# Kernel tuning notes

Hardware: AMD Instinct MI355X
Metric: run time of the kernel (lower is better)

The kernel has to match this reference:

```python
import jax, jax.numpy as jnp
import numpy as np


def bitnet_quantize(w):
    # scale = mean(|w|) clamped; ternary round of centered/scaled weights; STE
    scale = jnp.maximum(jnp.mean(jnp.abs(w)), 1e-8)
    w_centered = w - jnp.mean(w)
    w_bin = jnp.round(jnp.clip(w_centered / scale, -1.0, 1.0))
    w_q = jax.lax.stop_gradient(w_bin - w) + w  # forward: w_bin, grad: identity
    return w_q, scale


def setup_inputs() -> dict:
    key = jax.random.key(0)
    kx, kr, ki, kj, kk = jax.random.split(key, 5)
    B, S, F = 4, 4096, 2048
    C = F // 4  # 512 quaternion channels
    init_std = 0.02
    return {
        "x": jax.random.normal(kx, (B, S, F), dtype=jnp.float32),
        "r_weight": jax.random.normal(kr, (C, C), dtype=jnp.float32) * init_std,
        "i_weight": jax.random.normal(ki, (C, C), dtype=jnp.float32) * init_std,
        "j_weight": jax.random.normal(kj, (C, C), dtype=jnp.float32) * init_std,
        "k_weight": jax.random.normal(kk, (C, C), dtype=jnp.float32) * init_std,
        "bias": jnp.zeros((F,), dtype=jnp.float32),
    }


def reference(x, r_weight, i_weight, j_weight, k_weight, bias):
    # eval path of QuatBitLinear: ternary-quantize all 4 weights, shared scale
    r_w, s1 = bitnet_quantize(r_weight)
    i_w, s2 = bitnet_quantize(i_weight)
    j_w, s3 = bitnet_quantize(j_weight)
    k_w, s4 = bitnet_quantize(k_weight)
    scale = (s1 + s2 + s3 + s4) / 4.0

    r_in, i_in, j_in, k_in = jnp.split(x, 4, axis=-1)  # each [B,S,C]

    def lin(v, w):  # F.linear: v @ w.T
        return jnp.einsum('bsc,oc->bso', v, w)

    r_out = lin(r_in, r_w) - lin(i_in, i_w) - lin(j_in, j_w) - lin(k_in, k_w)
    i_out = lin(r_in, i_w) + lin(i_in, r_w) + lin(j_in, k_w) - lin(k_in, j_w)
    j_out = lin(r_in, j_w) - lin(i_in, k_w) + lin(j_in, r_w) + lin(k_in, i_w)
    k_out = lin(r_in, k_w) + lin(i_in, j_w) - lin(j_in, i_w) + lin(k_in, r_w)

    out = jnp.concatenate([r_out, i_out, j_out, k_out], axis=-1)
    out = out + bias  # bias added BEFORE scaling, as in the torch code
    return out * scale * 0.5
```

## Files before the change

### kernel.cpp

```cpp
#include <hip/hip_runtime.h>
#include <hip/hip_bf16.h>
#include <stdint.h>

typedef __attribute__((ext_vector_type(8))) short short8;
typedef __attribute__((ext_vector_type(4))) float f32x4;
typedef __attribute__((ext_vector_type(4))) float float4v;
typedef __attribute__((ext_vector_type(4))) unsigned short ushort4v;

static constexpr int C = 512;
static constexpr int F = 2048;
static constexpr int NW = C * C;

__device__ inline unsigned short f2bf(float f) {
    union { float f; unsigned int u; } cv;
    cv.f = f;
    unsigned int r = cv.u + 0x7fffu + ((cv.u >> 16) & 1u);
    return (unsigned short)(r >> 16);
}

__global__ void qb_sums(const float* __restrict__ w0, const float* __restrict__ w1,
                        const float* __restrict__ w2, const float* __restrict__ w3,
                        double* __restrict__ sums) {
    int wid = blockIdx.x >> 6;
    int chunk = blockIdx.x & 63;
    const float* wsel = (wid == 0) ? w0 : (wid == 1) ? w1 : (wid == 2) ? w2 : w3;
    const float* p = wsel + chunk * (NW / 64);
    double sa = 0.0, sv = 0.0;
    for (int i = threadIdx.x; i < (NW / 64) / 4; i += 256) {
        float4v v = ((const float4v*)p)[i];
        sa += (double)fabsf(v.x) + fabsf(v.y) + fabsf(v.z) + fabsf(v.w);
        sv += (double)v.x + v.y + v.z + v.w;
    }
    for (int off = 32; off; off >>= 1) {
        sa += __shfl_down(sa, off);
        sv += __shfl_down(sv, off);
    }
    __shared__ double red[8];
    int wv = threadIdx.x >> 6;
    if ((threadIdx.x & 63) == 0) { red[wv] = sa; red[4 + wv] = sv; }
    __syncthreads();
    if (threadIdx.x == 0) {
        double tsa = red[0] + red[1] + red[2] + red[3];
        double tsv = red[4] + red[5] + red[6] + red[7];
        atomicAdd(&sums[wid * 2 + 0], tsa);
        atomicAdd(&sums[wid * 2 + 1], tsv);
    }
}

__global__ void qb_build(const float* __restrict__ w0, const float* __restrict__ w1,
                         const float* __restrict__ w2, const float* __restrict__ w3,
                         const double* __restrict__ sums, unsigned short* __restrict__ Wb) {
    int wid = blockIdx.x >> 7;
    int t = (blockIdx.x & 127) * 256 + threadIdx.x;
    int o = t >> 6;
    int c0 = (t & 63) << 3;
    const float sgn[4][4] = {{ 1.f, 1.f, 1.f, 1.f},
                             {-1.f, 1.f, 1.f,-1.f},
                             {-1.f,-1.f, 1.f, 1.f},
                             {-1.f, 1.f,-1.f, 1.f}};
    const float* wptr[4] = {w0, w1, w2, w3};
    float mf = (float)(sums[wid * 2 + 1] * (1.0 / NW));
    float scf = fmaxf((float)(sums[wid * 2 + 0] * (1.0 / NW)), 1e-8f);
    const float* w = wptr[wid] + o * C + c0;
    float4v va = ((const float4v*)w)[0];
    float4v vb = ((const float4v*)w)[1];
    float q[8];
#pragma unroll
    for (int e = 0; e < 4; ++e) {
        q[e]     = rintf(fminf(fmaxf((va[e] - mf) / scf, -1.f), 1.f));
        q[4 + e] = rintf(fminf(fmaxf((vb[e] - mf) / scf, -1.f), 1.f));
    }
#pragma unroll
    for (int p = 0; p < 4; ++p) {
        int qb = p ^ wid;
        float s = sgn[wid][p];
        short8 v;
#pragma unroll
        for (int e = 0; e < 8; ++e) v[e] = (short)f2bf(s * q[e]);
        *(short8*)&Wb[(size_t)(p * C + o) * F + qb * C + c0] = v;
    }
}

__global__ void qb_convert(const float* __restrict__ X, unsigned short* __restrict__ Xb, int n8) {
    int stride = gridDim.x * blockDim.x;
    for (int i = blockIdx.x * blockDim.x + threadIdx.x; i < n8; i += stride) {
        float4v a = ((const float4v*)X)[2 * i];
        float4v b = ((const float4v*)X)[2 * i + 1];
        short8 h;
        h[0] = (short)f2bf(a[0]); h[1] = (short)f2bf(a[1]);
        h[2] = (short)f2bf(a[2]); h[3] = (short)f2bf(a[3]);
        h[4] = (short)f2bf(b[0]); h[5] = (short)f2bf(b[1]);
        h[6] = (short)f2bf(b[2]); h[7] = (short)f2bf(b[3]);
        ((short8*)Xb)[i] = h;
    }
}

__global__ __launch_bounds__(512, 2) void qb_gemm256(
    const unsigned short* __restrict__ A,
    const unsigned short* __restrict__ B,
    const float* __restrict__ bias, const double* __restrict__ sums,
    float* __restrict__ out) {
    constexpr int K = F, N = F, BK = 64, NT = K / BK;
    __shared__ unsigned short As[2][256 * 64];
    __shared__ unsigned short Bs[2][256 * 64];

    const int tid = threadIdx.x;
    const int lane = tid & 63;
    const int w = tid >> 6;
    const int wm = w >> 2, wn = w & 3;

    const int nbn = N / 256;
    const int nwg = gridDim.x;
    const int bid = blockIdx.x;
    const int swz = (bid & 7) * (nwg >> 3) + (bid >> 3);
    const int bm = swz / nbn, bn = swz % nbn;
    const int brow = bm * 256, bcol = bn * 256;

    const int frow = lane & 15;
    const int fk = (lane >> 4) << 3;

    auto stage = [&](const unsigned short* __restrict__ gbase, int growbase,
                     unsigned short* ldsbase, int h, int kt) {
        int ktw = kt & (NT - 1);
#pragma unroll
        for (int l = 0; l < 2; ++l) {
            int boff = h * 16384 + (w * 2 + l) * 1024 + lane * 16;
            int e = boff >> 1;
            int r = e >> 6, c = e & 63;
            int csrc = c ^ ((r & 7) << 3);
            const unsigned short* src = gbase + (size_t)(growbase + r) * K + ktw * BK + csrc;
            __builtin_amdgcn_global_load_lds(
                (const __attribute__((address_space(1))) void*)src,
                (__attribute__((address_space(3))) void*)((char*)ldsbase + boff),
                16, 0, 0);
        }
    };
    auto rdA = [&](int buf, int mh, int ks, int mi) -> short8 {
        int r = mh * 128 + wm * 64 + mi * 16 + frow;
        int cs = (ks * 32 + fk) ^ ((r & 7) << 3);
        return *(const short8*)&As[buf][r * 64 + cs];
    };
    auto rdB = [&](int buf, int nh, int ks, int ni) -> short8 {
        int r = nh * 128 + wn * 32 + ni * 16 + frow;
        int cs = (ks * 32 + fk) ^ ((r & 7) << 3);
        return *(const short8*)&Bs[buf][r * 64 + cs];
    };

    f32x4 acc[2][4][2][2];
#pragma unroll
    for (int a0 = 0; a0 < 2; ++a0)
#pragma unroll
        for (int a1 = 0; a1 < 4; ++a1)
#pragma unroll
            for (int a2 = 0; a2 < 2; ++a2)
#pragma unroll
                for (int a3 = 0; a3 < 2; ++a3) acc[a0][a1][a2][a3] = (f32x4){0.f, 0.f, 0.f, 0.f};

    unsigned short* A0p = &As[0][0];
    unsigned short* A1p = &As[1][0];
    unsigned short* B0p = &Bs[0][0];
    unsigned short* B1p = &Bs[1][0];

    stage(B, bcol, B0p, 0, 0);
    stage(A, brow, A0p, 0, 0);
    stage(A, brow, A0p, 1, 0);
    stage(B, bcol, B0p, 1, 0);
    stage(B, bcol, B1p, 0, 1);
    stage(A, brow, A1p, 0, 1);
    asm volatile("s_waitcnt vmcnt(4)" ::: "memory");
    __builtin_amdgcn_s_barrier();

#define QB_PHASE(BUFC, MH, NH, STAGE_STMT, TILE_END)                                   \
    {                                                                                  \
        short8 af[2][4], bq[2][2];                                                     \
        _Pragma("unroll") for (int ks = 0; ks < 2; ++ks) {                             \
            _Pragma("unroll") for (int mi = 0; mi < 4; ++mi)                           \
                af[ks][mi] = rdA(BUFC, MH, ks, mi);                                    \
            _Pragma("unroll") for (int ni = 0; ni < 2; ++ni)                           \
                bq[ks][ni] = rdB(BUFC, NH, ks, ni);                                    \
        }                                                                              \
        STAGE_STMT;                                                                    \
        __builtin_amdgcn_s_barrier();                                                  \
        asm volatile("s_waitcnt lgkmcnt(0)" ::: "memory");                             \
        __builtin_amdgcn_sched_barrier(0);                                             \
        __builtin_amdgcn_s_setprio(1);                                                 \
        _Pragma("unroll") for (int ks = 0; ks < 2; ++ks)                               \
            _Pragma("unroll") for (int mi = 0; mi < 4; ++mi)                           \
                _Pragma("unroll") for (int ni = 0; ni < 2; ++ni)                       \
                    acc[MH][mi][NH][ni] = __builtin_amdgcn_mfma_f32_16x16x32_bf16(     \
                        af[ks][mi], bq[ks][ni], acc[MH][mi][NH][ni], 0, 0, 0);         \
        __builtin_amdgcn_s_setprio(0);                                                 \
        TILE_END;                                                                      \
        __builtin_amdgcn_s_barrier();                                                  \
    }

    for (int it = 0; it < NT / 2; ++it) {
        int kt0 = 2 * it;
        QB_PHASE(0, 0, 0, stage(A, brow, A1p, 1, kt0 + 1), ((void)0))
        QB_PHASE(0, 1, 0, stage(B, bcol, B1p, 1, kt0 + 1), ((void)0))
        QB_PHASE(0, 0, 1, stage(B, bcol, B0p, 0, kt0 + 2), ((void)0))
        QB_PHASE(0, 1, 1, stage(A, brow, A0p, 0, kt0 + 2),
                 asm volatile("s_waitcnt vmcnt(4)" ::: "memory"))
        QB_PHASE(1, 0, 0, stage(A, brow, A0p, 1, kt0 + 2), ((void)0))
        QB_PHASE(1, 1, 0, stage(B, bcol, B0p, 1, kt0 + 2), ((void)0))
        QB_PHASE(1, 0, 1, stage(B, bcol, B1p, 0, kt0 + 3), ((void)0))
        QB_PHASE(1, 1, 1, stage(A, brow, A1p, 0, kt0 + 3),
                 asm volatile("s_waitcnt vmcnt(4)" ::: "memory"))
    }
#undef QB_PHASE

    float s0 = fmaxf((float)(sums[0] * (1.0 / NW)), 1e-8f);
    float s1 = fmaxf((float)(sums[2] * (1.0 / NW)), 1e-8f);
    float s2 = fmaxf((float)(sums[4] * (1.0 / NW)), 1e-8f);
    float s3 = fmaxf((float)(sums[6] * (1.0 / NW)), 1e-8f);
    float mul = (s0 + s1 + s2 + s3) * 0.25f * 0.5f;

#pragma unroll
    for (int mh = 0; mh < 2; ++mh)
#pragma unroll
        for (int nh = 0; nh < 2; ++nh)
#pragma unroll
            for (int ni = 0; ni < 2; ++ni) {
                int gcol = bcol + nh * 128 + wn * 32 + ni * 16 + frow;
                float bv = bias[gcol];
#pragma unroll
                for (int mi = 0; mi < 4; ++mi) {
                    int gr0 = brow + mh * 128 + wm * 64 + mi * 16 + ((lane >> 4) << 2);
#pragma unroll
                    for (int j = 0; j < 4; ++j)
                        out[(size_t)(gr0 + j) * N + gcol] = (acc[mh][mi][nh][ni][j] + bv) * mul;
                }
            }
}

__global__ __launch_bounds__(256) void qb_gemm(
    const float* __restrict__ X, const unsigned short* __restrict__ Wb,
    const float* __restrict__ bias, const double* __restrict__ sums,
    float* __restrict__ out, int M) {
    constexpr int Kd = F, Nd = F;
    __shared__ unsigned short As[128 * 32];
    __shared__ unsigned short Bs[128 * 32];
    const int t = threadIdx.x;
    const int lane = t & 63, wv = t >> 6;
    const int nbn = Nd / 128;
    const int nwg = gridDim.x;
    const int bid = blockIdx.x;
    const int swz = (bid & 7) * (nwg >> 3) + (bid >> 3);
    const int bm = swz / nbn, bn = swz % nbn;
    const int brow = bm * 128, bcol = bn * 128;
    const int wr = wv >> 1, wc = wv & 1;
    const int frow = lane & 15;
    const int k8 = (lane >> 4) << 3;
    f32x4 acc[4][4];
#pragma unroll
    for (int i = 0; i < 4; ++i)
#pragma unroll
        for (int j = 0; j < 4; ++j) acc[i][j] = (f32x4){0.f, 0.f, 0.f, 0.f};
    const int ar = t >> 3;
    const int ac = (t & 7) << 2;
    for (int kk = 0; kk < Kd; kk += 32) {
#pragma unroll
        for (int is = 0; is < 2; ++is) {
            int idx = is * 2048 + t * 8;
            int row = idx >> 5, col = idx & 31;
            const unsigned short* src = &Wb[(size_t)(bcol + row) * Kd + kk + col];
            __builtin_amdgcn_global_load_lds(
                (const __attribute__((address_space(1))) void*)src,
                (__attribute__((address_space(3))) void*)&Bs[idx], 16, 0, 0);
        }
#pragma unroll
        for (int it = 0; it < 4; ++it) {
            int row = it * 32 + ar;
            float4v v = *(const float4v*)&X[(size_t)(brow + row) * Kd + kk + ac];
            ushort4v h;
            h[0] = f2bf(v[0]); h[1] = f2bf(v[1]); h[2] = f2bf(v[2]); h[3] = f2bf(v[3]);
            *(ushort4v*)&As[row * 32 + ac] = h;
        }
        __syncthreads();
        short8 a[4], b[4];
#pragma unroll
        for (int mi = 0; mi < 4; ++mi)
            a[mi] = *(const short8*)&As[(wr * 64 + mi * 16 + frow) * 32 + k8];
#pragma unroll
        for (int ni = 0; ni < 4; ++ni)
            b[ni] = *(const short8*)&Bs[(wc * 64 + ni * 16 + frow) * 32 + k8];
#pragma unroll
        for (int mi = 0; mi < 4; ++mi)
#pragma unroll
            for (int ni = 0; ni < 4; ++ni)
                acc[mi][ni] = __builtin_amdgcn_mfma_f32_16x16x32_bf16(
                    a[mi], b[ni], acc[mi][ni], 0, 0, 0);
        __syncthreads();
    }
    float s0 = fmaxf((float)(sums[0] * (1.0 / NW)), 1e-8f);
    float s1 = fmaxf((float)(sums[2] * (1.0 / NW)), 1e-8f);
    float s2 = fmaxf((float)(sums[4] * (1.0 / NW)), 1e-8f);
    float s3 = fmaxf((float)(sums[6] * (1.0 / NW)), 1e-8f);
    float mul = (s0 + s1 + s2 + s3) * 0.25f * 0.5f;
#pragma unroll
    for (int ni = 0; ni < 4; ++ni) {
        int gcol = bcol + wc * 64 + ni * 16 + frow;
        float bv = bias[gcol];
#pragma unroll
        for (int mi = 0; mi < 4; ++mi) {
            int growb = brow + wr * 64 + mi * 16 + ((lane >> 4) << 2);
#pragma unroll
            for (int j = 0; j < 4; ++j)
                out[(size_t)(growb + j) * Nd + gcol] = (acc[mi][ni][j] + bv) * mul;
        }
    }
}

extern "C" void kernel_launch(void* const* d_in, const int* in_sizes, int n_in,
                              void* d_out, int out_size, void* d_ws, size_t ws_size,
                              hipStream_t stream) {
    const float* x    = (const float*)d_in[0];
    const float* wr_  = (const float*)d_in[1];
    const float* wi_  = (const float*)d_in[2];
    const float* wj_  = (const float*)d_in[3];
    const float* wk_  = (const float*)d_in[4];
    const float* bias = (const float*)d_in[5];
    float* out = (float*)d_out;
    const int M = in_sizes[0] / F;

    const size_t WB_OFF = 4096;
    const size_t XB_OFF = WB_OFF + (size_t)F * F * 2;
    const size_t NEED   = XB_OFF + (size_t)M * F * 2;

    double* sums = (double*)d_ws;
    unsigned short* Wb = (unsigned short*)((char*)d_ws + WB_OFF);

    hipMemsetAsync(d_ws, 0, 64, stream);
    qb_sums<<<256, 256, 0, stream>>>(wr_, wi_, wj_, wk_, sums);
    qb_build<<<512, 256, 0, stream>>>(wr_, wi_, wj_, wk_, sums, Wb);

    if (ws_size >= NEED && (M % 256) == 0) {
        unsigned short* Xb = (unsigned short*)((char*)d_ws + XB_OFF);
        qb_convert<<<2048, 256, 0, stream>>>(x, Xb, (M * F) / 8);
        const int grid = (M / 256) * (F / 256);
        qb_gemm256<<<grid, 512, 0, stream>>>(Xb, Wb, bias, sums, out);
    } else {
        const int grid = (M / 128) * (F / 128);
        qb_gemm<<<grid, 256, 0, stream>>>(x, Wb, bias, sums, out, M);
    }
}
```

Baseline: 412.0 us.

## Fuse weight stats into convert kernel, drop memset/atomics, reschedule GEMM fragment loads

Merges the weight-statistics reduction into the X-to-bf16 conversion launch as extra blocks. Each block writes its partial sums to its own slot, so the memset and double atomics go away. qb_build now reduces the partials itself and writes the final scales. Inside the 256x256 GEMM, B fragments are held across phases and the next tile's B0 fragments are prefetched at the end of each tile, which cuts LDS reads per phase and reorders staging. The added register pressure and the reordered barriers could hurt occupancy or scheduling.

```diff
diff --git a/kernel.cpp b/kernel.cpp
--- a/kernel.cpp
+++ b/kernel.cpp
@@ -18,72 +18,37 @@
     return (unsigned short)(r >> 16);
 }
 
-__global__ void qb_sums(const float* __restrict__ w0, const float* __restrict__ w1,
+__global__ void qb_prep(const float* __restrict__ X, unsigned short* __restrict__ Xb, int n8,
+                        const float* __restrict__ w0, const float* __restrict__ w1,
                         const float* __restrict__ w2, const float* __restrict__ w3,
-                        double* __restrict__ sums) {
-    int wid = blockIdx.x >> 6;
-    int chunk = blockIdx.x & 63;
-    const float* wsel = (wid == 0) ? w0 : (wid == 1) ? w1 : (wid == 2) ? w2 : w3;
-    const float* p = wsel + chunk * (NW / 64);
-    double sa = 0.0, sv = 0.0;
-    for (int i = threadIdx.x; i < (NW / 64) / 4; i += 256) {
-        float4v v = ((const float4v*)p)[i];
-        sa += (double)fabsf(v.x) + fabsf(v.y) + fabsf(v.z) + fabsf(v.w);
-        sv += (double)v.x + v.y + v.z + v.w;
-    }
-    for (int off = 32; off; off >>= 1) {
-        sa += __shfl_down(sa, off);
-        sv += __shfl_down(sv, off);
-    }
+                        double* __restrict__ part) {
     __shared__ double red[8];
-    int wv = threadIdx.x >> 6;
-    if ((threadIdx.x & 63) == 0) { red[wv] = sa; red[4 + wv] = sv; }
-    __syncthreads();
-    if (threadIdx.x == 0) {
-        double tsa = red[0] + red[1] + red[2] + red[3];
-        double tsv = red[4] + red[5] + red[6] + red[7];
-        atomicAdd(&sums[wid * 2 + 0], tsa);
-        atomicAdd(&sums[wid * 2 + 1], tsv);
-    }
-}
-
-__global__ void qb_build(const float* __restrict__ w0, const float* __restrict__ w1,
-                         const float* __restrict__ w2, const float* __restrict__ w3,
-                         const double* __restrict__ sums, unsigned short* __restrict__ Wb) {
-    int wid = blockIdx.x >> 7;
-    int t = (blockIdx.x & 127) * 256 + threadIdx.x;
-    int o = t >> 6;
-    int c0 = (t & 63) << 3;
-    const float sgn[4][4] = {{ 1.f, 1.f, 1.f, 1.f},
-                             {-1.f, 1.f, 1.f,-1.f},
-                             {-1.f,-1.f, 1.f, 1.f},
-                             {-1.f, 1.f,-1.f, 1.f}};
-    const float* wptr[4] = {w0, w1, w2, w3};
-    float mf = (float)(sums[wid * 2 + 1] * (1.0 / NW));
-    float scf = fmaxf((float)(sums[wid * 2 + 0] * (1.0 / NW)), 1e-8f);
-    const float* w = wptr[wid] + o * C + c0;
-    float4v va = ((const float4v*)w)[0];
-    float4v vb = ((const float4v*)w)[1];
-    float q[8];
-#pragma unroll
-    for (int e = 0; e < 4; ++e) {
-        q[e]     = rintf(fminf(fmaxf((va[e] - mf) / scf, -1.f), 1.f));
-        q[4 + e] = rintf(fminf(fmaxf((vb[e] - mf) / scf, -1.f), 1.f));
-    }
-#pragma unroll
-    for (int p = 0; p < 4; ++p) {
-        int qb = p ^ wid;
-        float s = sgn[wid][p];
-        short8 v;
-#pragma unroll
-        for (int e = 0; e < 8; ++e) v[e] = (short)f2bf(s * q[e]);
-        *(short8*)&Wb[(size_t)(p * C + o) * F + qb * C + c0] = v;
-    }
-}
-
-__global__ void qb_convert(const float* __restrict__ X, unsigned short* __restrict__ Xb, int n8) {
-    int stride = gridDim.x * blockDim.x;
-    for (int i = blockIdx.x * blockDim.x + threadIdx.x; i < n8; i += stride) {
+    if (blockIdx.x >= 2048) {
+        int b = blockIdx.x - 2048;
+        int wid = b >> 6, chunk = b & 63;
+        const float* wsel = (wid == 0) ? w0 : (wid == 1) ? w1 : (wid == 2) ? w2 : w3;
+        const float* p = wsel + chunk * (NW / 64);
+        double sa = 0.0, sv = 0.0;
+        for (int i = threadIdx.x; i < (NW / 64) / 4; i += 256) {
+            float4v v = ((const float4v*)p)[i];
+            sa += (double)fabsf(v.x) + fabsf(v.y) + fabsf(v.z) + fabsf(v.w);
+            sv += (double)v.x + v.y + v.z + v.w;
+        }
+        for (int off = 32; off; off >>= 1) {
+            sa += __shfl_down(sa, off);
+            sv += __shfl_down(sv, off);
+        }
+        int wv = threadIdx.x >> 6;
+        if ((threadIdx.x & 63) == 0) { red[wv] = sa; red[4 + wv] = sv; }
+        __syncthreads();
+        if (threadIdx.x == 0) {
+            part[b * 2 + 0] = red[0] + red[1] + red[2] + red[3];
+            part[b * 2 + 1] = red[4] + red[5] + red[6] + red[7];
+        }
+        return;
+    }
+    int stride = 2048 * 256;
+    for (int i = blockIdx.x * 256 + threadIdx.x; i < n8; i += stride) {
         float4v a = ((const float4v*)X)[2 * i];
         float4v b = ((const float4v*)X)[2 * i + 1];
         short8 h;
@@ -95,10 +60,53 @@
     }
 }
 
+__global__ void qb_build(const float* __restrict__ w0, const float* __restrict__ w1,
+                         const float* __restrict__ w2, const float* __restrict__ w3,
+                         const double* __restrict__ part, unsigned short* __restrict__ Wb,
+                         double* __restrict__ finals) {
+    int wid = blockIdx.x >> 7;
+    int t = (blockIdx.x & 127) * 256 + threadIdx.x;
+    int o = t >> 6;
+    int c0 = (t & 63) << 3;
+    double sa = 0.0, sv = 0.0;
+#pragma unroll
+    for (int i = 0; i < 64; ++i) {
+        sa += part[(wid * 64 + i) * 2 + 0];
+        sv += part[(wid * 64 + i) * 2 + 1];
+    }
+    float mf = (float)(sv * (1.0 / NW));
+    float scf = fmaxf((float)(sa * (1.0 / NW)), 1e-8f);
+    if ((blockIdx.x & 127) == 0 && threadIdx.x == 0) finals[wid] = (double)scf;
+
+    const float sgn[4][4] = {{ 1.f, 1.f, 1.f, 1.f},
+                             {-1.f, 1.f, 1.f,-1.f},
+                             {-1.f,-1.f, 1.f, 1.f},
+                             {-1.f, 1.f,-1.f, 1.f}};
+    const float* wptr[4] = {w0, w1, w2, w3};
+    const float* w = wptr[wid] + o * C + c0;
+    float4v va = ((const float4v*)w)[0];
+    float4v vb = ((const float4v*)w)[1];
+    float q[8];
+#pragma unroll
+    for (int e = 0; e < 4; ++e) {
+        q[e]     = rintf(fminf(fmaxf((va[e] - mf) / scf, -1.f), 1.f));
+        q[4 + e] = rintf(fminf(fmaxf((vb[e] - mf) / scf, -1.f), 1.f));
+    }
+#pragma unroll
+    for (int p = 0; p < 4; ++p) {
+        int qb = p ^ wid;
+        float s = sgn[wid][p];
+        short8 v;
+#pragma unroll
+        for (int e = 0; e < 8; ++e) v[e] = (short)f2bf(s * q[e]);
+        *(short8*)&Wb[(size_t)(p * C + o) * F + qb * C + c0] = v;
+    }
+}
+
 __global__ __launch_bounds__(512, 2) void qb_gemm256(
     const unsigned short* __restrict__ A,
     const unsigned short* __restrict__ B,
-    const float* __restrict__ bias, const double* __restrict__ sums,
+    const float* __restrict__ bias, const double* __restrict__ finals,
     float* __restrict__ out) {
     constexpr int K = F, N = F, BK = 64, NT = K / BK;
     __shared__ unsigned short As[2][256 * 64];
@@ -156,64 +164,82 @@
 #pragma unroll
                 for (int a3 = 0; a3 < 2; ++a3) acc[a0][a1][a2][a3] = (f32x4){0.f, 0.f, 0.f, 0.f};
 
-    unsigned short* A0p = &As[0][0];
-    unsigned short* A1p = &As[1][0];
-    unsigned short* B0p = &Bs[0][0];
-    unsigned short* B1p = &Bs[1][0];
-
-    stage(B, bcol, B0p, 0, 0);
-    stage(A, brow, A0p, 0, 0);
-    stage(A, brow, A0p, 1, 0);
-    stage(B, bcol, B0p, 1, 0);
-    stage(B, bcol, B1p, 0, 1);
-    stage(A, brow, A1p, 0, 1);
+    stage(B, bcol, &Bs[0][0], 0, 0);
+    stage(A, brow, &As[0][0], 0, 0);
+    stage(A, brow, &As[0][0], 1, 0);
+    stage(B, bcol, &Bs[0][0], 1, 0);
+    stage(B, bcol, &Bs[1][0], 0, 1);
+    stage(A, brow, &As[1][0], 0, 1);
     asm volatile("s_waitcnt vmcnt(4)" ::: "memory");
     __builtin_amdgcn_s_barrier();
 
-#define QB_PHASE(BUFC, MH, NH, STAGE_STMT, TILE_END)                                   \
-    {                                                                                  \
-        short8 af[2][4], bq[2][2];                                                     \
-        _Pragma("unroll") for (int ks = 0; ks < 2; ++ks) {                             \
-            _Pragma("unroll") for (int mi = 0; mi < 4; ++mi)                           \
-                af[ks][mi] = rdA(BUFC, MH, ks, mi);                                    \
+    short8 af[2][4], b0[2][2], b1[2][2];
+#pragma unroll
+    for (int ks = 0; ks < 2; ++ks)
+#pragma unroll
+        for (int ni = 0; ni < 2; ++ni) b0[ks][ni] = rdB(0, 0, ks, ni);
+
+#define QB_MFMA(MH, NH, BB)                                                            \
+    _Pragma("unroll") for (int ks = 0; ks < 2; ++ks)                                   \
+        _Pragma("unroll") for (int mi = 0; mi < 4; ++mi)                               \
             _Pragma("unroll") for (int ni = 0; ni < 2; ++ni)                           \
-                bq[ks][ni] = rdB(BUFC, NH, ks, ni);                                    \
-        }                                                                              \
-        STAGE_STMT;                                                                    \
-        __builtin_amdgcn_s_barrier();                                                  \
-        asm volatile("s_waitcnt lgkmcnt(0)" ::: "memory");                             \
-        __builtin_amdgcn_sched_barrier(0);                                             \
-        __builtin_amdgcn_s_setprio(1);                                                 \
-        _Pragma("unroll") for (int ks = 0; ks < 2; ++ks)                               \
-            _Pragma("unroll") for (int mi = 0; mi < 4; ++mi)                           \
-                _Pragma("unroll") for (int ni = 0; ni < 2; ++ni)                       \
-                    acc[MH][mi][NH][ni] = __builtin_amdgcn_mfma_f32_16x16x32_bf16(     \
-                        af[ks][mi], bq[ks][ni], acc[MH][mi][NH][ni], 0, 0, 0);         \
-        __builtin_amdgcn_s_setprio(0);                                                 \
-        TILE_END;                                                                      \
-        __builtin_amdgcn_s_barrier();                                                  \
-    }
+                acc[MH][mi][NH][ni] = __builtin_amdgcn_mfma_f32_16x16x32_bf16(         \
+                    af[ks][mi], BB[ks][ni], acc[MH][mi][NH][ni], 0, 0, 0);
+
+#define QB_TILE(CB, KT)                                                                \
+                                           \
+    _Pragma("unroll") for (int ks = 0; ks < 2; ++ks)                                   \
+        _Pragma("unroll") for (int mi = 0; mi < 4; ++mi) af[ks][mi] = rdA(CB, 0, ks, mi); \
+    stage(A, brow, &As[1 - (CB)][0], 1, (KT) + 1);                                     \
+    __builtin_amdgcn_s_barrier();                                                      \
+    asm volatile("s_waitcnt lgkmcnt(0)" ::: "memory");                                 \
+    __builtin_amdgcn_sched_barrier(0);                                                 \
+    __builtin_amdgcn_s_setprio(1);                                                     \
+    QB_MFMA(0, 0, b0)                                                                  \
+    __builtin_amdgcn_s_setprio(0);                                                     \
+    __builtin_amdgcn_s_barrier();                                                      \
+                                             \
+    _Pragma("unroll") for (int ks = 0; ks < 2; ++ks)                                   \
+        _Pragma("unroll") for (int ni = 0; ni < 2; ++ni) b1[ks][ni] = rdB(CB, 1, ks, ni); \
+    stage(B, bcol, &Bs[1 - (CB)][0], 1, (KT) + 1);                                     \
+    __builtin_amdgcn_s_barrier();                                                      \
+    asm volatile("s_waitcnt lgkmcnt(0)" ::: "memory");                                 \
+    __builtin_amdgcn_sched_barrier(0);                                                 \
+    __builtin_amdgcn_s_setprio(1);                                                     \
+    QB_MFMA(0, 1, b1)                                                                  \
+    __builtin_amdgcn_s_setprio(0);                                                     \
+    __builtin_amdgcn_s_barrier();                                                      \
+                                             \
+    _Pragma("unroll") for (int ks = 0; ks < 2; ++ks)                                   \
+        _Pragma("unroll") for (int mi = 0; mi < 4; ++mi) af[ks][mi] = rdA(CB, 1, ks, mi); \
+    stage(B, bcol, &Bs[CB][0], 0, (KT) + 2);                                           \
+    __builtin_amdgcn_s_barrier();                                                      \
+    asm volatile("s_waitcnt lgkmcnt(0)" ::: "memory");                                 \
+    __builtin_amdgcn_sched_barrier(0);                                                 \
+    __builtin_amdgcn_s_setprio(1);                                                     \
+    QB_MFMA(1, 1, b1)                                                                  \
+    __builtin_amdgcn_s_setprio(0);                                                     \
+    __builtin_amdgcn_s_barrier();                                                      \
+          \
+    stage(A, brow, &As[CB][0], 0, (KT) + 2);                                           \
+    __builtin_amdgcn_s_barrier();                                                      \
+    __builtin_amdgcn_s_setprio(1);                                                     \
+    QB_MFMA(1, 0, b0)                                                                  \
+    __builtin_amdgcn_s_setprio(0);                                                     \
+    asm volatile("s_waitcnt vmcnt(4)" ::: "memory");                                   \
+    _Pragma("unroll") for (int ks = 0; ks < 2; ++ks)                                   \
+        _Pragma("unroll") for (int ni = 0; ni < 2; ++ni) b0[ks][ni] = rdB(1 - (CB), 0, ks, ni); \
+    __builtin_amdgcn_s_barrier();
 
     for (int it = 0; it < NT / 2; ++it) {
         int kt0 = 2 * it;
-        QB_PHASE(0, 0, 0, stage(A, brow, A1p, 1, kt0 + 1), ((void)0))
-        QB_PHASE(0, 1, 0, stage(B, bcol, B1p, 1, kt0 + 1), ((void)0))
-        QB_PHASE(0, 0, 1, stage(B, bcol, B0p, 0, kt0 + 2), ((void)0))
-        QB_PHASE(0, 1, 1, stage(A, brow, A0p, 0, kt0 + 2),
-                 asm volatile("s_waitcnt vmcnt(4)" ::: "memory"))
-        QB_PHASE(1, 0, 0, stage(A, brow, A0p, 1, kt0 + 2), ((void)0))
-        QB_PHASE(1, 1, 0, stage(B, bcol, B0p, 1, kt0 + 2), ((void)0))
-        QB_PHASE(1, 0, 1, stage(B, bcol, B1p, 0, kt0 + 3), ((void)0))
-        QB_PHASE(1, 1, 1, stage(A, brow, A1p, 0, kt0 + 3),
-                 asm volatile("s_waitcnt vmcnt(4)" ::: "memory"))
-    }
-#undef QB_PHASE
-
-    float s0 = fmaxf((float)(sums[0] * (1.0 / NW)), 1e-8f);
-    float s1 = fmaxf((float)(sums[2] * (1.0 / NW)), 1e-8f);
-    float s2 = fmaxf((float)(sums[4] * (1.0 / NW)), 1e-8f);
-    float s3 = fmaxf((float)(sums[6] * (1.0 / NW)), 1e-8f);
-    float mul = (s0 + s1 + s2 + s3) * 0.25f * 0.5f;
+        QB_TILE(0, kt0)
+        QB_TILE(1, kt0 + 1)
+    }
+#undef QB_TILE
+#undef QB_MFMA
+
+    float mul = (float)((finals[0] + finals[1] + finals[2] + finals[3]) * (0.25 * 0.5));
 
 #pragma unroll
     for (int mh = 0; mh < 2; ++mh)
@@ -235,7 +261,7 @@
 
 __global__ __launch_bounds__(256) void qb_gemm(
     const float* __restrict__ X, const unsigned short* __restrict__ Wb,
-    const float* __restrict__ bias, const double* __restrict__ sums,
+    const float* __restrict__ bias, const double* __restrict__ finals,
     float* __restrict__ out, int M) {
     constexpr int Kd = F, Nd = F;
     __shared__ unsigned short As[128 * 32];
@@ -292,11 +318,7 @@
                     a[mi], b[ni], acc[mi][ni], 0, 0, 0);
         __syncthreads();
     }
-    float s0 = fmaxf((float)(sums[0] * (1.0 / NW)), 1e-8f);
-    float s1 = fmaxf((float)(sums[2] * (1.0 / NW)), 1e-8f);
-    float s2 = fmaxf((float)(sums[4] * (1.0 / NW)), 1e-8f);
-    float s3 = fmaxf((float)(sums[6] * (1.0 / NW)), 1e-8f);
-    float mul = (s0 + s1 + s2 + s3) * 0.25f * 0.5f;
+    float mul = (float)((finals[0] + finals[1] + finals[2] + finals[3]) * (0.25 * 0.5));
 #pragma unroll
     for (int ni = 0; ni < 4; ++ni) {
         int gcol = bcol + wc * 64 + ni * 16 + frow;
@@ -323,24 +345,27 @@
     float* out = (float*)d_out;
     const int M = in_sizes[0] / F;
 
-    const size_t WB_OFF = 4096;
-    const size_t XB_OFF = WB_OFF + (size_t)F * F * 2;
-    const size_t NEED   = XB_OFF + (size_t)M * F * 2;
-
-    double* sums = (double*)d_ws;
+    const size_t FIN_OFF = 4096;
+    const size_t WB_OFF  = 8192;
+    const size_t XB_OFF  = WB_OFF + (size_t)F * F * 2;
+    const size_t NEED    = XB_OFF + (size_t)M * F * 2;
+
+    double* part   = (double*)d_ws;
+    double* finals = (double*)((char*)d_ws + FIN_OFF);
     unsigned short* Wb = (unsigned short*)((char*)d_ws + WB_OFF);
-
-    hipMemsetAsync(d_ws, 0, 64, stream);
-    qb_sums<<<256, 256, 0, stream>>>(wr_, wi_, wj_, wk_, sums);
-    qb_build<<<512, 256, 0, stream>>>(wr_, wi_, wj_, wk_, sums, Wb);
-
-    if (ws_size >= NEED && (M % 256) == 0) {
-        unsigned short* Xb = (unsigned short*)((char*)d_ws + XB_OFF);
-        qb_convert<<<2048, 256, 0, stream>>>(x, Xb, (M * F) / 8);
+    unsigned short* Xb = (unsigned short*)((char*)d_ws + XB_OFF);
+
+    const bool fast = (ws_size >= NEED) && (M % 256) == 0;
+
+    qb_prep<<<2304, 256, 0, stream>>>(x, Xb, fast ? (M * F) / 8 : 0,
+                                      wr_, wi_, wj_, wk_, part);
+    qb_build<<<512, 256, 0, stream>>>(wr_, wi_, wj_, wk_, part, Wb, finals);
+
+    if (fast) {
         const int grid = (M / 256) * (F / 256);
-        qb_gemm256<<<grid, 512, 0, stream>>>(Xb, Wb, bias, sums, out);
+        qb_gemm256<<<grid, 512, 0, stream>>>(Xb, Wb, bias, finals, out);
     } else {
         const int grid = (M / 128) * (F / 128);
-        qb_gemm<<<grid, 256, 0, stream>>>(x, Wb, bias, sums, out, M);
-    }
-}
+        qb_gemm<<<grid, 256, 0, stream>>>(x, Wb, bias, finals, out, M);
+    }
+}
```

Measured after the change: 387.6 us. 5.9% less time.
